# Kernel tuning notes

Measured on AMD Instinct MI355X. Metric: run time of the kernel, lower is better.

Reference implementation:

```python
import jax, jax.numpy as jnp
import numpy as np

D, H, DK = 512, 8, 64
SCALE = 1.5 / 1.0  # gamma/tau, schedule='const'
NEG = -1e30


def _cross(x_q, x_kv, mask_kv, Wq, Wk, Wv, scale):
    # x_q: [B,Tq,D], x_kv: [B,Tk,D], mask_kv: [B,Tk] (1=keep, 0=mask)
    B, Tq, _ = x_q.shape
    Tk = x_kv.shape[1]
    q = (x_q @ Wq.T).reshape(B, Tq, H, DK).transpose(0, 2, 1, 3)
    k = (x_kv @ Wk.T).reshape(B, Tk, H, DK).transpose(0, 2, 1, 3)
    v = (x_kv @ Wv.T).reshape(B, Tk, H, DK).transpose(0, 2, 1, 3)
    logits = jnp.einsum('bhqd,bhkd->bhqk', q, k) * (scale / jnp.sqrt(jnp.float32(DK)))
    if mask_kv is not None:
        logits = jnp.where(mask_kv[:, None, None, :] == 0, NEG, logits)
    attn = jax.nn.softmax(logits, axis=-1)
    out = jnp.einsum('bhqk,bhkd->bhqd', attn, v)
    return out.transpose(0, 2, 1, 3).reshape(B, Tq, D)


def setup_inputs() -> dict:
    key = jax.random.key(0)
    ks = jax.random.split(key, 12)
    B, T = 4, 2048
    inp = {
        'skel_seq': jax.random.normal(ks[0], (B, T, D), jnp.float32),
        'sens_seq': jax.random.normal(ks[1], (B, T, D), jnp.float32),
        'mask_skel': jax.random.randint(ks[2], (B, T), 0, 2, jnp.int32),
        'mask_sens': jax.random.randint(ks[3], (B, T), 0, 2, jnp.int32),
    }
    s = 1.0 / np.sqrt(D)
    names = ['Wq_s2e', 'Wk_e', 'Wv_e', 'Wq_e2s', 'Wk_s', 'Wv_s', 'Wo_s', 'Wo_e']
    for i, n in enumerate(names):
        inp[n] = jax.random.normal(ks[4 + i], (D, D), jnp.float32) * s
    return inp


def reference(skel_seq, sens_seq, mask_skel, mask_sens,
              Wq_s2e, Wk_e, Wv_e, Wq_e2s, Wk_s, Wv_s, Wo_s, Wo_e):
    # skel queries attend over sensor keys/values
    s2e = _cross(skel_seq, sens_seq, mask_sens, Wq_s2e, Wk_e, Wv_e, SCALE) @ Wo_e.T
    # sensor queries attend over skeleton keys/values
    e2s = _cross(sens_seq, skel_seq, mask_skel, Wq_e2s, Wk_s, Wv_s, SCALE) @ Wo_s.T
    return (e2s, s2e)
```

## Files before the change

### kernel.cpp

```cpp
#include <hip/hip_runtime.h>
#include <hip/hip_bf16.h>

#define T_SEQ 2048
#define N_TOK 4194304
#define W_ELEM 262144


typedef float f32x4  __attribute__((ext_vector_type(4)));
typedef short bf16x8 __attribute__((ext_vector_type(8)));

#define SCALE_Q 0.27050532f

__device__ __forceinline__ unsigned short f2b(float f) {
    __hip_bfloat16 h = __float2bfloat16(f);
    return *reinterpret_cast<unsigned short*>(&h);
}

__device__ __forceinline__ int pack2bf(float lo, float hi) {
    return ((int)f2b(hi) << 16) | (int)f2b(lo);
}

__device__ __forceinline__ bf16x8 ldg8(const unsigned short* p) {
    union { int4 i; bf16x8 b; } u;
    u.i = *reinterpret_cast<const int4*>(p);
    return u.b;
}

__device__ __forceinline__ float fexp2(float x) {
#if __has_builtin(__builtin_amdgcn_exp2f)
    return __builtin_amdgcn_exp2f(x);
#else
    return exp2f(x);
#endif
}

typedef unsigned int u32_g __attribute__((address_space(1)));
typedef unsigned int u32_l __attribute__((address_space(3)));
__device__ __forceinline__ void gload_lds16(const void* g, void* l) {
    __builtin_amdgcn_global_load_lds((const u32_g*)g, (u32_l*)l, 16, 0, 0);
}

__global__ __launch_bounds__(256)
void prep_bias(const int* __restrict__ ms, const int* __restrict__ mk,
               float* __restrict__ dst)
{
    const int i = (blockIdx.x * 256 + threadIdx.x) * 8;
    const int* m = (i >> 13) ? mk : ms;
    const int rem = i & 8191;
    const int4 a = *reinterpret_cast<const int4*>(&m[rem]);
    const int4 b = *reinterpret_cast<const int4*>(&m[rem + 4]);
    float4 f0, f1;
    f0.x = a.x ? 0.0f : -3e38f; f0.y = a.y ? 0.0f : -3e38f;
    f0.z = a.z ? 0.0f : -3e38f; f0.w = a.w ? 0.0f : -3e38f;
    f1.x = b.x ? 0.0f : -3e38f; f1.y = b.y ? 0.0f : -3e38f;
    f1.z = b.z ? 0.0f : -3e38f; f1.w = b.w ? 0.0f : -3e38f;
    *reinterpret_cast<float4*>(&dst[i])     = f0;
    *reinterpret_cast<float4*>(&dst[i + 4]) = f1;
}

__global__ __launch_bounds__(256)
void to_bf16(const float* __restrict__ s0, const float* __restrict__ s1,
             const float* __restrict__ w0, const float* __restrict__ w1,
             const float* __restrict__ w2, const float* __restrict__ w3,
             const float* __restrict__ w4, const float* __restrict__ w5,
             unsigned short* __restrict__ dst)
{
    const int bid = blockIdx.x;
    int y, x;
    if (bid < 4096) { y = bid >> 11; x = bid & 2047; }
    else { const int t = bid - 4096; y = 2 + (t >> 7); x = t & 127; }
    const float* src;
    size_t off;
    switch (y) {
        case 0: src = s0; off = 0;      break;
        case 1: src = s1; off = N_TOK;  break;
        case 2: src = w0; off = 2 * (size_t)N_TOK;              break;
        case 3: src = w1; off = 2 * (size_t)N_TOK + 1 * W_ELEM; break;
        case 4: src = w2; off = 2 * (size_t)N_TOK + 2 * W_ELEM; break;
        case 5: src = w3; off = 2 * (size_t)N_TOK + 3 * W_ELEM; break;
        case 6: src = w4; off = 2 * (size_t)N_TOK + 4 * W_ELEM; break;
        default: src = w5; off = 2 * (size_t)N_TOK + 5 * W_ELEM; break;
    }
    const int idx = (x * 256 + threadIdx.x) * 8;
    const float4 a = *reinterpret_cast<const float4*>(src + idx);
    const float4 b = *reinterpret_cast<const float4*>(src + idx + 4);
    int4 o;
    o.x = pack2bf(a.x, a.y); o.y = pack2bf(a.z, a.w);
    o.z = pack2bf(b.x, b.y); o.w = pack2bf(b.z, b.w);
    *reinterpret_cast<int4*>(dst + off + idx) = o;
}

#define MF_SETUP                                                               \
    __shared__ short Asm[64][72];                                              \
    __shared__ short Wsm[64][72];                                              \
    const int tid  = threadIdx.x;                                              \
    const int lane = tid & 63;                                                 \
    const int w4   = tid >> 6;                                                 \
    const int nl   = lane & 15;                                                \
    const int quad = lane >> 4;                                                \
    const int n0 = blockIdx.x * 64;                                            \
    const int m0 = blockIdx.y * 64;                                            \
    const int arow = tid >> 2;                                                 \
    const int acol = (tid & 3) * 16;                                           \
    f32x4 acc[4] = {};

#define MF_WRITE_W                                                             \
    {                                                                          \
        int4 x;                                                                \
        x.x = pack2bf(wv[0].x, wv[0].y); x.y = pack2bf(wv[0].z, wv[0].w);      \
        x.z = pack2bf(wv[1].x, wv[1].y); x.w = pack2bf(wv[1].z, wv[1].w);      \
        *reinterpret_cast<int4*>(&Wsm[arow][acol]) = x;                        \
        x.x = pack2bf(wv[2].x, wv[2].y); x.y = pack2bf(wv[2].z, wv[2].w);      \
        x.z = pack2bf(wv[3].x, wv[3].y); x.w = pack2bf(wv[3].z, wv[3].w);      \
        *reinterpret_cast<int4*>(&Wsm[arow][acol + 8]) = x;                    \
    }

#define MF_MMA_LOOP                                                            \
    _Pragma("unroll")                                                          \
    for (int kc = 0; kc < 2; ++kc) {                                           \
        const bf16x8 a = *reinterpret_cast<const bf16x8*>(                     \
            &Asm[w4 * 16 + nl][kc * 32 + quad * 8]);                           \
        _Pragma("unroll")                                                      \
        for (int c = 0; c < 4; ++c) {                                          \
            const bf16x8 bf = *reinterpret_cast<const bf16x8*>(                \
                &Wsm[c * 16 + nl][kc * 32 + quad * 8]);                        \
            acc[c] = __builtin_amdgcn_mfma_f32_16x16x32_bf16(a, bf, acc[c],    \
                                                             0, 0, 0);         \
        }                                                                      \
    }

#define MF_CWRITE_PROJ                                                         \
    if (!trans) {                                                              \
        _Pragma("unroll")                                                      \
        for (int c = 0; c < 4; ++c)                                            \
            _Pragma("unroll")                                                  \
            for (int r = 0; r < 4; ++r)                                        \
                C[(size_t)(m0 + w4 * 16 + quad * 4 + r) * 512 + n0 + c * 16 + nl] = \
                    f2b(acc[c][r] * alpha);                                    \
    } else {                                                                   \
        const int b  = m0 >> 11;                                               \
        const int t0 = (m0 & 2047) + w4 * 16 + quad * 4;                       \
        _Pragma("unroll")                                                      \
        for (int c = 0; c < 4; ++c) {                                          \
            const int n = n0 + c * 16 + nl;                                    \
            ushort4 o;                                                         \
            o.x = f2b(acc[c][0]);                                              \
            o.y = f2b(acc[c][1]);                                              \
            o.z = f2b(acc[c][2]);                                              \
            o.w = f2b(acc[c][3]);                                              \
            *reinterpret_cast<ushort4*>(C + (size_t)(b * 512 + n) * T_SEQ + t0) = o; \
        }                                                                      \
    }

__global__ __launch_bounds__(256)
void proj_all(const float* __restrict__ skel, const float* __restrict__ sens,
              const float* __restrict__ Wq1, const float* __restrict__ Wk1,
              const float* __restrict__ Wv1, const float* __restrict__ Wq2,
              const float* __restrict__ Wk2, const float* __restrict__ Wv2,
              unsigned short* __restrict__ Q1, unsigned short* __restrict__ K1,
              unsigned short* __restrict__ Vt1, unsigned short* __restrict__ Q2,
              unsigned short* __restrict__ K2, unsigned short* __restrict__ Vt2,
              int zbase)
{
    const int z = zbase + blockIdx.z;
    const float* A; const float* W; unsigned short* C;
    float alpha = 1.0f; bool trans = false;
    switch (z) {
        case 0:  A = skel; W = Wq1; C = Q1; alpha = SCALE_Q; break;
        case 1:  A = sens; W = Wk1; C = K1; break;
        case 2:  A = sens; W = Wv1; C = Vt1; trans = true; break;
        case 3:  A = sens; W = Wq2; C = Q2; alpha = SCALE_Q; break;
        case 4:  A = skel; W = Wk2; C = K2; break;
        default: A = skel; W = Wv2; C = Vt2; trans = true; break;
    }

    MF_SETUP
    const float* ap = A + (size_t)(m0 + arow) * 512 + acol;
    const float* wp = W + (size_t)(n0 + arow) * 512 + acol;
    float4 av[4], wv[4];
    #pragma unroll
    for (int j = 0; j < 4; ++j) {
        av[j] = *reinterpret_cast<const float4*>(ap + 4 * j);
        wv[j] = *reinterpret_cast<const float4*>(wp + 4 * j);
    }
    for (int it = 0; it < 8; ++it) {
        __syncthreads();
        {
            int4 x;
            x.x = pack2bf(av[0].x, av[0].y); x.y = pack2bf(av[0].z, av[0].w);
            x.z = pack2bf(av[1].x, av[1].y); x.w = pack2bf(av[1].z, av[1].w);
            *reinterpret_cast<int4*>(&Asm[arow][acol]) = x;
            x.x = pack2bf(av[2].x, av[2].y); x.y = pack2bf(av[2].z, av[2].w);
            x.z = pack2bf(av[3].x, av[3].y); x.w = pack2bf(av[3].z, av[3].w);
            *reinterpret_cast<int4*>(&Asm[arow][acol + 8]) = x;
        }
        MF_WRITE_W
        __syncthreads();
        if (it < 7) {
            const float* apn = ap + (it + 1) * 64;
            const float* wpn = wp + (it + 1) * 64;
            #pragma unroll
            for (int j = 0; j < 4; ++j) {
                av[j] = *reinterpret_cast<const float4*>(apn + 4 * j);
                wv[j] = *reinterpret_cast<const float4*>(wpn + 4 * j);
            }
        }
        MF_MMA_LOOP
    }
    MF_CWRITE_PROJ
}

__global__ __launch_bounds__(256, 2)
void proj_fused(const unsigned short* __restrict__ skb,
                const unsigned short* __restrict__ snb,
                const unsigned short* __restrict__ wball,
                unsigned short* __restrict__ Q1, unsigned short* __restrict__ K1,
                unsigned short* __restrict__ Vt1, unsigned short* __restrict__ Q2,
                unsigned short* __restrict__ K2, unsigned short* __restrict__ Vt2)
{
    __shared__ __align__(16) char smem[65536];
    short (*Al)[128][64] = reinterpret_cast<short (*)[128][64]>(smem);
    short (*Wl)[128][64] = reinterpret_cast<short (*)[128][64]>(smem + 32768);

    const int o   = blockIdx.x;
    const int wg  = (o & 7) * 192 + (o >> 3);
    const int z   = wg >> 8;
    const int idx = wg & 255;
    const int nh  = idx & 3;
    const int mt  = idx >> 2;

    const unsigned short* A = (z == 0 || z >= 4) ? skb : snb;
    const unsigned short* W = wball + (size_t)z * W_ELEM;
    unsigned short* C;
    switch (z) {
        case 0: C = Q1;  break;
        case 1: C = K1;  break;
        case 2: C = Vt1; break;
        case 3: C = Q2;  break;
        case 4: C = K2;  break;
        default: C = Vt2; break;
    }
    const bool trans = (z == 2 || z == 5);
    const float alpha = (z == 0 || z == 3) ? SCALE_Q : 1.0f;

    const int tid  = threadIdx.x;
    const int w    = tid >> 6;
    const int wr   = w >> 1;
    const int wc   = w & 1;
    const int lane = tid & 63;
    const int nl   = lane & 15;
    const int quad = lane >> 4;
    const int r8   = lane >> 3;
    const int cg   = (lane & 7) ^ r8;

    const int m0g = mt * 128;
    const int n0  = nh * 128;

    const unsigned short* Ab = A + (size_t)m0g * 512 + cg * 8;
    const unsigned short* Wb = W + (size_t)n0  * 512 + cg * 8;

    f32x4 acc[4][4] = {};

    auto stage = [&](int it, int buf) {
        const int k0 = it * 64;
        #pragma unroll
        for (int g = 0; g < 4; ++g) {
            const int rr = w * 32 + g * 8;
            gload_lds16(Ab + (size_t)(rr + r8) * 512 + k0, &Al[buf][rr][0]);
            gload_lds16(Wb + (size_t)(rr + r8) * 512 + k0, &Wl[buf][rr][0]);
        }
    };

    stage(0, 0);
    asm volatile("s_waitcnt vmcnt(0)" ::: "memory");
    __syncthreads();

    const int sw = nl & 7;
    for (int it = 0; it < 8; ++it) {
        const int buf = it & 1;
        if (it < 7) stage(it + 1, buf ^ 1);
        #pragma unroll
        for (int kc = 0; kc < 2; ++kc) {
            bf16x8 a[4], bb[4];
            #pragma unroll
            for (int am = 0; am < 4; ++am)
                a[am] = *reinterpret_cast<const bf16x8*>(
                    &Al[buf][wr * 64 + am * 16 + nl][((kc * 4 + quad) ^ sw) * 8]);
            #pragma unroll
            for (int bn = 0; bn < 4; ++bn)
                bb[bn] = *reinterpret_cast<const bf16x8*>(
                    &Wl[buf][wc * 64 + bn * 16 + nl][((kc * 4 + quad) ^ sw) * 8]);
            #pragma unroll
            for (int am = 0; am < 4; ++am)
                #pragma unroll
                for (int bn = 0; bn < 4; ++bn)
                    acc[am][bn] = __builtin_amdgcn_mfma_f32_16x16x32_bf16(
                        a[am], bb[bn], acc[am][bn], 0, 0, 0);
        }
        asm volatile("s_waitcnt vmcnt(0)" ::: "memory");
        __syncthreads();
    }

    if (!trans) {
        short (*Cl)[132] = reinterpret_cast<short (*)[132]>(smem);
        #pragma unroll
        for (int am = 0; am < 4; ++am)
            #pragma unroll
            for (int bn = 0; bn < 4; ++bn)
                #pragma unroll
                for (int r = 0; r < 4; ++r)
                    Cl[wr * 64 + am * 16 + quad * 4 + r][wc * 64 + bn * 16 + nl] =
                        (short)f2b(acc[am][bn][r] * alpha);
        __syncthreads();
        const int lr = tid >> 1;
        const int ch = (tid & 1) * 64;
        unsigned short* cp = C + (size_t)(m0g + lr) * 512 + n0 + ch;
        #pragma unroll
        for (int j = 0; j < 8; ++j)
            *reinterpret_cast<int4*>(cp + j * 8) =
                *reinterpret_cast<const int4*>(&Cl[lr][ch + j * 8]);
    } else {
        short (*Tl)[132] = reinterpret_cast<short (*)[132]>(smem);
        #pragma unroll
        for (int am = 0; am < 4; ++am)
            #pragma unroll
            for (int bn = 0; bn < 4; ++bn) {
                int* dst = reinterpret_cast<int*>(
                    &Tl[wc * 64 + bn * 16 + nl][wr * 64 + am * 16 + quad * 4]);
                dst[0] = pack2bf(acc[am][bn][0], acc[am][bn][1]);
                dst[1] = pack2bf(acc[am][bn][2], acc[am][bn][3]);
            }
        __syncthreads();
        const int bq = m0g >> 11;
        const int t0 = m0g & 2047;
        const int nr = tid >> 1;
        const int tc = (tid & 1) * 64;
        unsigned short* vp = C + (size_t)(bq * 512 + n0 + nr) * T_SEQ + t0 + tc;
        #pragma unroll
        for (int j = 0; j < 8; ++j)
            *reinterpret_cast<int4*>(vp + j * 8) =
                *reinterpret_cast<const int4*>(&Tl[nr][tc + j * 8]);
    }
}

__global__ __launch_bounds__(256, 2)
void out_fused(const unsigned short* __restrict__ AO1, const float* __restrict__ Wo1,
               float* __restrict__ C1,
               const unsigned short* __restrict__ AO2, const float* __restrict__ Wo2,
               float* __restrict__ C2)
{
    __shared__ __align__(16) char smem[67584];
    short (*Al)[128][64] = reinterpret_cast<short (*)[128][64]>(smem);
    short (*Wl)[128][64] = reinterpret_cast<short (*)[128][64]>(smem + 32768);

    const int o   = blockIdx.x;
    const int wg  = (o & 7) * 64 + (o >> 3);
    const int z   = wg >> 8;
    const int idx = wg & 255;
    const int nh  = idx & 3;
    const int mt  = idx >> 2;

    const unsigned short* A = z ? AO2 : AO1;
    const float* W = z ? Wo2 : Wo1;
    float* C = z ? C2 : C1;

    const int tid  = threadIdx.x;
    const int w    = tid >> 6;
    const int wr   = w >> 1;
    const int wc   = w & 1;
    const int lane = tid & 63;
    const int nl   = lane & 15;
    const int quad = lane >> 4;
    const int r8   = lane >> 3;
    const int cg   = (lane & 7) ^ r8;

    const int m0g = mt * 128;
    const int n0  = nh * 128;

    const unsigned short* Ab = A + (size_t)m0g * 512 + cg * 8;

    const int rw_ = tid >> 1;
    const int ch_ = (tid & 1) * 32;
    const int key = rw_ & 7;

    f32x4 acc[4][4] = {};
    float4 wreg[8];

    auto stageA = [&](int it, int buf) {
        const int k0 = it * 64;
        #pragma unroll
        for (int g = 0; g < 4; ++g) {
            const int rr = w * 32 + g * 8;
            gload_lds16(Ab + (size_t)(rr + r8) * 512 + k0, &Al[buf][rr][0]);
        }
    };
    auto wload = [&](int it) {
        const float* wp = W + (size_t)(n0 + rw_) * 512 + it * 64 + ch_;
        #pragma unroll
        for (int j = 0; j < 8; ++j)
            wreg[j] = *reinterpret_cast<const float4*>(wp + 4 * j);
    };
    auto wstore = [&](int buf) {
        #pragma unroll
        for (int j = 0; j < 8; ++j) {
            int2 pk;
            pk.x = pack2bf(wreg[j].x, wreg[j].y);
            pk.y = pack2bf(wreg[j].z, wreg[j].w);
            const int slot = ((tid & 1) * 4 + (j >> 1)) ^ key;
            *reinterpret_cast<int2*>(
                &Wl[buf][rw_][slot * 8 + (j & 1) * 4]) = pk;
        }
    };

    wload(0);
    stageA(0, 0);
    asm volatile("s_waitcnt vmcnt(0)" ::: "memory");
    wstore(0);
    __syncthreads();

    const int sw = nl & 7;
    for (int it = 0; it < 8; ++it) {
        const int buf = it & 1;
        if (it < 7) { stageA(it + 1, buf ^ 1); wload(it + 1); }
        #pragma unroll
        for (int kc = 0; kc < 2; ++kc) {
            bf16x8 a[4], bb[4];
            #pragma unroll
            for (int am = 0; am < 4; ++am)
                a[am] = *reinterpret_cast<const bf16x8*>(
                    &Al[buf][wr * 64 + am * 16 + nl][((kc * 4 + quad) ^ sw) * 8]);
            #pragma unroll
            for (int bn = 0; bn < 4; ++bn)
                bb[bn] = *reinterpret_cast<const bf16x8*>(
                    &Wl[buf][wc * 64 + bn * 16 + nl][((kc * 4 + quad) ^ sw) * 8]);
            #pragma unroll
            for (int am = 0; am < 4; ++am)
                #pragma unroll
                for (int bn = 0; bn < 4; ++bn)
                    acc[am][bn] = __builtin_amdgcn_mfma_f32_16x16x32_bf16(
                        a[am], bb[bn], acc[am][bn], 0, 0, 0);
        }
        asm volatile("s_waitcnt vmcnt(0)" ::: "memory");
        if (it < 7) wstore(buf ^ 1);
        __syncthreads();
    }

    float (*Cl)[132] = reinterpret_cast<float (*)[132]>(smem);
    #pragma unroll
    for (int am = 0; am < 4; ++am)
        #pragma unroll
        for (int bn = 0; bn < 4; ++bn)
            #pragma unroll
            for (int r = 0; r < 4; ++r)
                Cl[wr * 64 + am * 16 + quad * 4 + r][wc * 64 + bn * 16 + nl] =
                    acc[am][bn][r];
    __syncthreads();
    const int lr = tid >> 1;
    const int fc = (tid & 1) * 64;
    float* cp = C + (size_t)(m0g + lr) * 512 + n0 + fc;
    #pragma unroll
    for (int j = 0; j < 16; ++j)
        *reinterpret_cast<float4*>(cp + j * 4) =
            *reinterpret_cast<const float4*>(&Cl[lr][fc + j * 4]);
}

__global__ __launch_bounds__(256)
void out_proj(const unsigned short* __restrict__ AO1, const float* __restrict__ Wo1,
              float* __restrict__ C1,
              const unsigned short* __restrict__ AO2, const float* __restrict__ Wo2,
              float* __restrict__ C2, int zbase)
{
    const int z = zbase + blockIdx.z;
    const unsigned short* A = z ? AO2 : AO1;
    const float* W = z ? Wo2 : Wo1;
    float* C = z ? C2 : C1;

    MF_SETUP
    const unsigned short* ap = A + (size_t)(m0 + arow) * 512 + acol;
    const float* wp = W + (size_t)(n0 + arow) * 512 + acol;
    int4 ai[2];
    float4 wv[4];
    ai[0] = *reinterpret_cast<const int4*>(ap);
    ai[1] = *reinterpret_cast<const int4*>(ap + 8);
    #pragma unroll
    for (int j = 0; j < 4; ++j)
        wv[j] = *reinterpret_cast<const float4*>(wp + 4 * j);
    for (int it = 0; it < 8; ++it) {
        __syncthreads();
        *reinterpret_cast<int4*>(&Asm[arow][acol])     = ai[0];
        *reinterpret_cast<int4*>(&Asm[arow][acol + 8]) = ai[1];
        MF_WRITE_W
        __syncthreads();
        if (it < 7) {
            const unsigned short* apn = ap + (it + 1) * 64;
            const float* wpn = wp + (it + 1) * 64;
            ai[0] = *reinterpret_cast<const int4*>(apn);
            ai[1] = *reinterpret_cast<const int4*>(apn + 8);
            #pragma unroll
            for (int j = 0; j < 4; ++j)
                wv[j] = *reinterpret_cast<const float4*>(wpn + 4 * j);
        }
        MF_MMA_LOOP
    }
    #pragma unroll
    for (int c = 0; c < 4; ++c)
        #pragma unroll
        for (int r = 0; r < 4; ++r)
            C[(size_t)(m0 + w4 * 16 + quad * 4 + r) * 512 + n0 + c * 16 + nl] =
                acc[c][r];
}

__global__ __launch_bounds__(512)
void attn_mfma(const unsigned short* Q1x, const unsigned short* __restrict__ K1x,
               const unsigned short* __restrict__ V1x, const float* __restrict__ b1x,
               unsigned short* AO1x,
               const unsigned short* Q2x, const unsigned short* __restrict__ K2x,
               const unsigned short* __restrict__ V2x, const float* __restrict__ b2x,
               unsigned short* AO2x)
{
    __shared__ short Kl[2][64][64];
    __shared__ short Vl[2][64][64];
    __shared__ short Pl[8][16][64];

    const int dir = blockIdx.y >> 5;
    const unsigned short* Q  = dir ? Q2x : Q1x;
    const unsigned short* K  = dir ? K2x : K1x;
    const unsigned short* Vt = dir ? V2x : V1x;
    const float* biasD       = dir ? b2x : b1x;
    unsigned short* AO       = dir ? AO2x : AO1x;

    const int tid  = threadIdx.x;
    const int w    = tid >> 6;
    const int lane = tid & 63;
    const int nl   = lane & 15;
    const int quad = lane >> 4;
    const int qt = blockIdx.x;
    const int bh = blockIdx.y & 31;
    const int b = bh >> 3, h = bh & 7;
    const size_t tb = (size_t)b * (T_SEQ * 512);
    const float* biasB = biasD + b * T_SEQ;

    const int r8 = lane >> 3;
    const int cg = (lane & 7) ^ r8;
    const int sr = w * 8;

    const unsigned short* qp = Q + tb + (size_t)(qt * 128 + w * 16 + nl) * 512 + h * 64 + quad * 8;
    const bf16x8 qb0 = ldg8(qp);
    const bf16x8 qb1 = ldg8(qp + 32);

    float l_run = 0.0f;
    f32x4 o[4] = {};

    gload_lds16(K  + tb + (size_t)(sr + r8) * 512 + h * 64 + cg * 8, &Kl[0][sr][0]);
    gload_lds16(Vt + (size_t)(b * 512 + h * 64 + sr + r8) * T_SEQ + cg * 8, &Vl[0][sr][0]);
    asm volatile("s_waitcnt vmcnt(0)" ::: "memory");
    __syncthreads();

    const int swz = nl & 7;

    for (int kt = 0; kt < 32; ++kt) {
        const int cur = kt & 1;
        short (*Kb)[64] = Kl[cur];
        short (*Vb)[64] = Vl[cur];

        if (kt < 31) {
            short (*Kn)[64] = Kl[cur ^ 1];
            short (*Vn)[64] = Vl[cur ^ 1];
            gload_lds16(K  + tb + (size_t)((kt + 1) * 64 + sr + r8) * 512 + h * 64 + cg * 8, &Kn[sr][0]);
            gload_lds16(Vt + (size_t)(b * 512 + h * 64 + sr + r8) * T_SEQ + (size_t)(kt + 1) * 64 + cg * 8, &Vn[sr][0]);
        }

        float p[4][4];
        #pragma unroll
        for (int s = 0; s < 4; ++s) {
            const bf16x8 k0 = *reinterpret_cast<const bf16x8*>(&Kb[s * 16 + nl][(quad ^ swz) * 8]);
            const bf16x8 k1 = *reinterpret_cast<const bf16x8*>(&Kb[s * 16 + nl][((4 + quad) ^ swz) * 8]);
            const float4 bb = *reinterpret_cast<const float4*>(
                &biasB[kt * 64 + s * 16 + quad * 4]);
            f32x4 z = {bb.x, bb.y, bb.z, bb.w};
            z = __builtin_amdgcn_mfma_f32_16x16x32_bf16(k0, qb0, z, 0, 0, 0);
            z = __builtin_amdgcn_mfma_f32_16x16x32_bf16(k1, qb1, z, 0, 0, 0);
            p[s][0] = fexp2(z[0]);
            p[s][1] = fexp2(z[1]);
            p[s][2] = fexp2(z[2]);
            p[s][3] = fexp2(z[3]);
            l_run += p[s][0] + p[s][1] + p[s][2] + p[s][3];
        }

        #pragma unroll
        for (int s = 0; s < 4; ++s) {
            int2 pk;
            pk.x = pack2bf(p[s][0], p[s][1]);
            pk.y = pack2bf(p[s][2], p[s][3]);
            const int slot = (2 * s + (quad >> 1)) ^ swz;
            *reinterpret_cast<int2*>(&Pl[w][nl][slot * 8 + (quad & 1) * 4]) = pk;
        }

        const bf16x8 pa0 = *reinterpret_cast<const bf16x8*>(&Pl[w][nl][(quad ^ swz) * 8]);
        const bf16x8 pa1 = *reinterpret_cast<const bf16x8*>(&Pl[w][nl][((4 + quad) ^ swz) * 8]);
        __builtin_amdgcn_s_setprio(1);
        #pragma unroll
        for (int sd = 0; sd < 4; ++sd) {
            const bf16x8 v0 = *reinterpret_cast<const bf16x8*>(&Vb[sd * 16 + nl][(quad ^ swz) * 8]);
            const bf16x8 v1 = *reinterpret_cast<const bf16x8*>(&Vb[sd * 16 + nl][((4 + quad) ^ swz) * 8]);
            o[sd] = __builtin_amdgcn_mfma_f32_16x16x32_bf16(v0, pa0, o[sd], 0, 0, 0);
            o[sd] = __builtin_amdgcn_mfma_f32_16x16x32_bf16(v1, pa1, o[sd], 0, 0, 0);
        }
        __builtin_amdgcn_s_setprio(0);

        asm volatile("s_waitcnt vmcnt(0)" ::: "memory");
        __syncthreads();
    }

    l_run += __shfl_xor(l_run, 16);
    l_run += __shfl_xor(l_run, 32);
    const float inv = 1.0f / l_run;
    unsigned short* ob = AO + tb + (size_t)(qt * 128 + w * 16 + nl) * 512 + h * 64 + quad * 4;
    #pragma unroll
    for (int sd = 0; sd < 4; ++sd) {
        ushort4 o4;
        o4.x = f2b(o[sd][0] * inv);
        o4.y = f2b(o[sd][1] * inv);
        o4.z = f2b(o[sd][2] * inv);
        o4.w = f2b(o[sd][3] * inv);
        *reinterpret_cast<ushort4*>(ob + sd * 16) = o4;
    }
}

extern "C" void kernel_launch(void* const* d_in, const int* in_sizes, int n_in,
                              void* d_out, int out_size, void* d_ws, size_t ws_size,
                              hipStream_t stream) {
    const float* skel = (const float*)d_in[0];
    const float* sens = (const float*)d_in[1];
    const int* mask_skel = (const int*)d_in[2];
    const int* mask_sens = (const int*)d_in[3];
    const float* Wq_s2e = (const float*)d_in[4];
    const float* Wk_e   = (const float*)d_in[5];
    const float* Wv_e   = (const float*)d_in[6];
    const float* Wq_e2s = (const float*)d_in[7];
    const float* Wk_s   = (const float*)d_in[8];
    const float* Wv_s   = (const float*)d_in[9];
    const float* Wo_s   = (const float*)d_in[10];
    const float* Wo_e   = (const float*)d_in[11];
    float* out = (float*)d_out;

    unsigned short* Q1 = (unsigned short*)d_ws;
    unsigned short* K1 = Q1 + N_TOK;
    unsigned short* V1 = K1 + N_TOK;

    const bool big = ws_size >= (size_t)6 * N_TOK * sizeof(unsigned short);

    if (big) {
        unsigned short* Q2 = V1 + N_TOK;
        unsigned short* K2 = Q2 + N_TOK;
        unsigned short* V2 = K2 + N_TOK;
        unsigned short* SC  = (unsigned short*)d_out;
        unsigned short* skb = SC;
        unsigned short* snb = SC + N_TOK;
        unsigned short* wb  = SC + 2 * (size_t)N_TOK;
        float* biasS = (float*)(SC + 2 * (size_t)N_TOK + 6 * W_ELEM);
        float* bias0 = biasS;
        float* bias1 = biasS + 4 * T_SEQ;
        prep_bias<<<dim3(8), 256, 0, stream>>>(mask_sens, mask_skel, biasS);
        to_bf16<<<dim3(4864), 256, 0, stream>>>(
            skel, sens, Wq_s2e, Wk_e, Wv_e, Wq_e2s, Wk_s, Wv_s, SC);
        proj_fused<<<dim3(1536), 256, 0, stream>>>(
            skb, snb, wb, Q1, K1, V1, Q2, K2, V2);
        attn_mfma<<<dim3(16, 64), 512, 0, stream>>>(
            Q1, K1, V1, bias0, Q1,
            Q2, K2, V2, bias1, Q2);
        out_fused<<<dim3(512), 256, 0, stream>>>(
            Q1, Wo_e, out + N_TOK, Q2, Wo_s, out);
    } else {
        float* bias0 = out;
        float* bias1 = out + 8192;
        prep_bias<<<dim3(8), 256, 0, stream>>>(mask_sens, mask_skel, bias0);
        proj_all<<<dim3(8, 128, 3), 256, 0, stream>>>(
            skel, sens, Wq_s2e, Wk_e, Wv_e, Wq_e2s, Wk_s, Wv_s,
            Q1, K1, V1, Q1, K1, V1, 0);
        attn_mfma<<<dim3(16, 32), 512, 0, stream>>>(
            Q1, K1, V1, bias0, Q1, Q1, K1, V1, bias0, Q1);
        out_proj<<<dim3(8, 128, 1), 256, 0, stream>>>(
            Q1, Wo_e, out + N_TOK, Q1, Wo_s, out, 0);
        proj_all<<<dim3(8, 128, 3), 256, 0, stream>>>(
            skel, sens, Wq_s2e, Wk_e, Wv_e, Wq_e2s, Wk_s, Wv_s,
            Q1, K1, V1, Q1, K1, V1, 3);
        attn_mfma<<<dim3(16, 32), 512, 0, stream>>>(
            Q1, K1, V1, bias1, Q1, Q1, K1, V1, bias1, Q1);
        out_proj<<<dim3(8, 128, 1), 256, 0, stream>>>(
            Q1, Wo_s, out, Q1, Wo_s, out, 1);
    }
}
```

Before: 300.9 us.

## Use nontemporal epilogue stores, pad LDS rows, split attention into two launches

Epilogue global stores in the projection and output kernels now use nontemporal stores, so write-once outputs are meant to bypass cache retention. LDS staging rows for the bf16 epilogue are padded from 132 to 136 shorts to change the bank mapping. The attention kernel drops its per-block direction select and is launched twice, once per direction, instead of once over a doubled grid. Two launches halve the blocks available per launch (512 each) and add launch overhead, which may reduce occupancy and overlap on the GPU.

```diff
diff --git a/kernel.cpp b/kernel.cpp
--- a/kernel.cpp
+++ b/kernel.cpp
@@ -8,6 +8,7 @@
 
 typedef float f32x4  __attribute__((ext_vector_type(4)));
 typedef short bf16x8 __attribute__((ext_vector_type(8)));
+typedef int   i32x4  __attribute__((ext_vector_type(4)));
 
 #define SCALE_Q 0.27050532f
 
@@ -32,6 +33,15 @@
 #else
     return exp2f(x);
 #endif
+}
+
+__device__ __forceinline__ void nt_store_i4(void* p, const void* src) {
+    __builtin_nontemporal_store(*reinterpret_cast<const i32x4*>(src),
+                                reinterpret_cast<i32x4*>(p));
+}
+__device__ __forceinline__ void nt_store_f4(void* p, const void* src) {
+    __builtin_nontemporal_store(*reinterpret_cast<const f32x4*>(src),
+                                reinterpret_cast<f32x4*>(p));
 }
 
 typedef unsigned int u32_g __attribute__((address_space(1)));
@@ -302,7 +312,7 @@
     }
 
     if (!trans) {
-        short (*Cl)[132] = reinterpret_cast<short (*)[132]>(smem);
+        short (*Cl)[136] = reinterpret_cast<short (*)[136]>(smem);
         #pragma unroll
         for (int am = 0; am < 4; ++am)
             #pragma unroll
@@ -317,10 +327,9 @@
         unsigned short* cp = C + (size_t)(m0g + lr) * 512 + n0 + ch;
         #pragma unroll
         for (int j = 0; j < 8; ++j)
-            *reinterpret_cast<int4*>(cp + j * 8) =
-                *reinterpret_cast<const int4*>(&Cl[lr][ch + j * 8]);
+            nt_store_i4(cp + j * 8, &Cl[lr][ch + j * 8]);
     } else {
-        short (*Tl)[132] = reinterpret_cast<short (*)[132]>(smem);
+        short (*Tl)[136] = reinterpret_cast<short (*)[136]>(smem);
         #pragma unroll
         for (int am = 0; am < 4; ++am)
             #pragma unroll
@@ -338,8 +347,7 @@
         unsigned short* vp = C + (size_t)(bq * 512 + n0 + nr) * T_SEQ + t0 + tc;
         #pragma unroll
         for (int j = 0; j < 8; ++j)
-            *reinterpret_cast<int4*>(vp + j * 8) =
-                *reinterpret_cast<const int4*>(&Tl[nr][tc + j * 8]);
+            nt_store_i4(vp + j * 8, &Tl[nr][tc + j * 8]);
     }
 }
 
@@ -460,8 +468,7 @@
     float* cp = C + (size_t)(m0g + lr) * 512 + n0 + fc;
     #pragma unroll
     for (int j = 0; j < 16; ++j)
-        *reinterpret_cast<float4*>(cp + j * 4) =
-            *reinterpret_cast<const float4*>(&Cl[lr][fc + j * 4]);
+        nt_store_f4(cp + j * 4, &Cl[lr][fc + j * 4]);
 }
 
 __global__ __launch_bounds__(256)
@@ -511,23 +518,13 @@
 }
 
 __global__ __launch_bounds__(512)
-void attn_mfma(const unsigned short* Q1x, const unsigned short* __restrict__ K1x,
-               const unsigned short* __restrict__ V1x, const float* __restrict__ b1x,
-               unsigned short* AO1x,
-               const unsigned short* Q2x, const unsigned short* __restrict__ K2x,
-               const unsigned short* __restrict__ V2x, const float* __restrict__ b2x,
-               unsigned short* AO2x)
+void attn_mfma(const unsigned short* Q, const unsigned short* __restrict__ K,
+               const unsigned short* __restrict__ Vt, const float* __restrict__ biasD,
+               unsigned short* AO)
 {
     __shared__ short Kl[2][64][64];
     __shared__ short Vl[2][64][64];
     __shared__ short Pl[8][16][64];
-
-    const int dir = blockIdx.y >> 5;
-    const unsigned short* Q  = dir ? Q2x : Q1x;
-    const unsigned short* K  = dir ? K2x : K1x;
-    const unsigned short* Vt = dir ? V2x : V1x;
-    const float* biasD       = dir ? b2x : b1x;
-    unsigned short* AO       = dir ? AO2x : AO1x;
 
     const int tid  = threadIdx.x;
     const int w    = tid >> 6;
@@ -666,9 +663,8 @@
             skel, sens, Wq_s2e, Wk_e, Wv_e, Wq_e2s, Wk_s, Wv_s, SC);
         proj_fused<<<dim3(1536), 256, 0, stream>>>(
             skb, snb, wb, Q1, K1, V1, Q2, K2, V2);
-        attn_mfma<<<dim3(16, 64), 512, 0, stream>>>(
-            Q1, K1, V1, bias0, Q1,
-            Q2, K2, V2, bias1, Q2);
+        attn_mfma<<<dim3(16, 32), 512, 0, stream>>>(Q1, K1, V1, bias0, Q1);
+        attn_mfma<<<dim3(16, 32), 512, 0, stream>>>(Q2, K2, V2, bias1, Q2);
         out_fused<<<dim3(512), 256, 0, stream>>>(
             Q1, Wo_e, out + N_TOK, Q2, Wo_s, out);
     } else {
@@ -678,15 +674,13 @@
         proj_all<<<dim3(8, 128, 3), 256, 0, stream>>>(
             skel, sens, Wq_s2e, Wk_e, Wv_e, Wq_e2s, Wk_s, Wv_s,
             Q1, K1, V1, Q1, K1, V1, 0);
-        attn_mfma<<<dim3(16, 32), 512, 0, stream>>>(
-            Q1, K1, V1, bias0, Q1, Q1, K1, V1, bias0, Q1);
+        attn_mfma<<<dim3(16, 32), 512, 0, stream>>>(Q1, K1, V1, bias0, Q1);
         out_proj<<<dim3(8, 128, 1), 256, 0, stream>>>(
             Q1, Wo_e, out + N_TOK, Q1, Wo_s, out, 0);
         proj_all<<<dim3(8, 128, 3), 256, 0, stream>>>(
             skel, sens, Wq_s2e, Wk_e, Wv_e, Wq_e2s, Wk_s, Wv_s,
             Q1, K1, V1, Q1, K1, V1, 3);
-        attn_mfma<<<dim3(16, 32), 512, 0, stream>>>(
-            Q1, K1, V1, bias1, Q1, Q1, K1, V1, bias1, Q1);
+        attn_mfma<<<dim3(16, 32), 512, 0, stream>>>(Q1, K1, V1, bias1, Q1);
         out_proj<<<dim3(8, 128, 1), 256, 0, stream>>>(
             Q1, Wo_s, out, Q1, Wo_s, out, 1);
     }
```

Result: slower. 432.9 us (+43.9%).
